# Optimization experiments

Measured on AMD Instinct MI355X. Metric: run time of the kernel, lower is better.

Reference implementation:

```python
import jax, jax.numpy as jnp
import numpy as np

RAD = 0.15          # sphere radius (init kwarg)
MIN_DIST = 2.0 * RAD  # two spheres collide when center distance < 2*rad


def setup_inputs() -> dict:
    key = jax.random.key(0)
    pos = jax.random.normal(key, (64, 1024, 3), dtype=jnp.float32)  # [T, N, 3]
    return {"pos": pos}


def reference(pos):
    """Sphere collision check equivalent to the sweep-and-prune CUDA kernel.

    The CUDA kernel sorts along one axis purely as an acceleration structure;
    the math it computes is: over all unordered robot pairs (i<j) at each
    timestep, a pair collides if ||p_i - p_j|| < 2*rad. Returns
      count: total number of colliding pairs (int)
      loss:  sum over colliding pairs of (2*rad - dist)^2 penetration penalty
    """
    T, N, _ = pos.shape
    diff = pos[:, :, None, :] - pos[:, None, :, :]          # [T, N, N, 3]
    dist2 = jnp.sum(diff * diff, axis=-1)                   # [T, N, N]
    iu = jnp.triu(jnp.ones((N, N), dtype=bool), k=1)        # i < j, exclude self
    colliding = iu[None, :, :] & (dist2 < MIN_DIST * MIN_DIST)
    # safe sqrt (diagonal / coincident points have dist2 == 0)
    safe_d2 = jnp.where(dist2 > 0.0, dist2, 1.0)
    dist = jnp.sqrt(safe_d2)
    pen = MIN_DIST - dist                                   # penetration depth
    loss = jnp.sum(jnp.where(colliding, pen * pen, 0.0))
    count = jnp.sum(colliding).astype(jnp.int32)
    return (count, loss)
```

## Files before the change

kernel.cpp:

```cpp
#include <hip/hip_runtime.h>
#include <math.h>

#define TN     64
#define NP     1024
#define RADIUS 0.15f
#define MIN_D  (2.0f * RADIUS)
#define R2     (MIN_D * MIN_D)

#define BLOCK  512
#define WAVES  (BLOCK / 64)
#define SPLIT  8
#define GI     16
#define NGRP   (NP / GI)
#define NBLK   (TN * SPLIT)
#define PPT    (NP / BLOCK)

#define NB     40
#define XMIN   (-6.0f)
#define INVW   3.3f

__launch_bounds__(BLOCK, 4)
__global__ void collide_kernel(const float* __restrict__ pos,
                               double* __restrict__ partial) {
    __shared__ float         shin[NP * 3];
    __shared__ float         shs [NP * 3];
    __shared__ unsigned int  hist[NB];
    __shared__ unsigned int  S[NB + 1];
    __shared__ unsigned char sbin[NP];

    const int t     = blockIdx.x / SPLIT;
    const int split = blockIdx.x % SPLIT;
    const int tid   = threadIdx.x;
    const int lane  = tid & 63;
    const int wave  = tid >> 6;

    const float4* p4  = (const float4*)(pos + (size_t)t * NP * 3);
    float4*       sh4 = (float4*)shin;
    for (int i = tid; i < NP * 3 / 4; i += BLOCK) sh4[i] = p4[i];
    if (tid < NB) hist[tid] = 0u;
    __syncthreads();

    int          bq[PPT];
    unsigned int rq[PPT];
    #pragma unroll
    for (int q = 0; q < PPT; ++q) {
        const int p = tid + q * BLOCK;
        const float x = shin[3 * p];
        int b = (int)((x - XMIN) * INVW);
        b = b < 0 ? 0 : (b > NB - 1 ? NB - 1 : b);
        bq[q] = b;
        rq[q] = atomicAdd(&hist[b], 1u);
    }
    __syncthreads();

    if (tid < 64) {
        unsigned int c    = (tid < NB) ? hist[tid] : 0u;
        unsigned int incl = c;
        #pragma unroll
        for (int d = 1; d < 64; d <<= 1) {
            const unsigned int y = __shfl_up(incl, d, 64);
            if (lane >= d) incl += y;
        }
        if (tid < NB) S[tid + 1] = incl;
        if (tid == 0) S[0] = 0u;
    }
    __syncthreads();

    #pragma unroll
    for (int q = 0; q < PPT; ++q) {
        const int p = tid + q * BLOCK;
        const unsigned int dst = S[bq[q]] + rq[q];
        shs[3 * dst + 0] = shin[3 * p + 0];
        shs[3 * dst + 1] = shin[3 * p + 1];
        shs[3 * dst + 2] = shin[3 * p + 2];
        sbin[dst] = (unsigned char)bq[q];
    }
    __syncthreads();

    unsigned int cnt  = 0;
    double       loss = 0.0;
    {
        const int g = wave * SPLIT + split;
        const int b = g * GI;

        float xi[GI], yi[GI], zi[GI];
        #pragma unroll
        for (int k = 0; k < GI; ++k) {
            xi[k] = shs[3 * (b + k) + 0];
            yi[k] = shs[3 * (b + k) + 1];
            zi[k] = shs[3 * (b + k) + 2];
        }
        #pragma unroll
        for (int k = 0; k < GI; ++k)
            asm volatile("" : "+v"(xi[k]), "+v"(yi[k]), "+v"(zi[k]));

        const int bb   = (int)sbin[b + GI - 1];
        const int jend = (int)S[(bb + 2 <= NB) ? (bb + 2) : NB];

        if (lane < GI - 1) {
            const int j = b + 1 + lane;
            const float xj = shs[3 * j], yj = shs[3 * j + 1], zj = shs[3 * j + 2];
            #pragma unroll
            for (int k = 0; k < GI; ++k) {
                if (k <= lane) {
                    const float dx = xi[k] - xj;
                    const float dy = yi[k] - yj;
                    const float dz = zi[k] - zj;
                    const float d2 = dx * dx + dy * dy + dz * dz;
                    if (d2 < R2) {
                        cnt++;
                        const float pen = MIN_D - __builtin_amdgcn_sqrtf(d2);
                        loss += (double)(pen * pen);
                    }
                }
            }
        }

        for (int j = b + GI + lane; j < jend; j += 64) {
            const float xj = shs[3 * j], yj = shs[3 * j + 1], zj = shs[3 * j + 2];
            #pragma unroll
            for (int k = 0; k < GI; ++k) {
                const float dx = xi[k] - xj;
                const float dy = yi[k] - yj;
                const float dz = zi[k] - zj;
                const float d2 = dx * dx + dy * dy + dz * dz;
                const bool hit = d2 < R2;
                cnt += hit ? 1u : 0u;
                if (hit) {
                    const float pen = MIN_D - __builtin_amdgcn_sqrtf(d2);
                    loss += (double)(pen * pen);
                }
            }
        }
    }

    float fcnt = (float)cnt;
    #pragma unroll
    for (int off = 32; off > 0; off >>= 1) {
        fcnt += __shfl_down(fcnt, off);
        loss += __shfl_down(loss, off);
    }
    __shared__ double cs[WAVES], ls[WAVES];
    if (lane == 0) { cs[wave] = (double)fcnt; ls[wave] = loss; }
    __syncthreads();
    if (tid == 0) {
        double c = 0.0, l = 0.0;
        #pragma unroll
        for (int w = 0; w < WAVES; ++w) { c += cs[w]; l += ls[w]; }
        partial[2 * blockIdx.x + 0] = c;
        partial[2 * blockIdx.x + 1] = l;
    }
}

__global__ void finalize_kernel(const double* __restrict__ partial,
                                float* __restrict__ out) {
    const int tid = threadIdx.x;
    double c = 0.0, l = 0.0;
    #pragma unroll
    for (int i = 0; i < NBLK / 256; ++i) {
        const double2 p = ((const double2*)partial)[tid + i * 256];
        c += p.x;
        l += p.y;
    }
    #pragma unroll
    for (int off = 32; off > 0; off >>= 1) {
        c += __shfl_down(c, off);
        l += __shfl_down(l, off);
    }
    __shared__ double cs[4], ls[4];
    const int wave = tid >> 6;
    if ((tid & 63) == 0) { cs[wave] = c; ls[wave] = l; }
    __syncthreads();
    if (tid == 0) {
        double ct = 0.0, lt = 0.0;
        #pragma unroll
        for (int w = 0; w < 4; ++w) { ct += cs[w]; lt += ls[w]; }
        out[0] = (float)ct;
        out[1] = (float)lt;
    }
}

extern "C" void kernel_launch(void* const* d_in, const int* in_sizes, int n_in,
                              void* d_out, int out_size, void* d_ws, size_t ws_size,
                              hipStream_t stream) {
    const float* pos     = (const float*)d_in[0];
    double*      partial = (double*)d_ws;
    float*       out     = (float*)d_out;

    collide_kernel<<<NBLK, BLOCK, 0, stream>>>(pos, partial);
    finalize_kernel<<<1, 256, 0, stream>>>(partial, out);
}
```

Measured before the change: 65.36 us.

## Use float accumulation, load positions into registers, and shrink finalize kernel

Loss is now accumulated in float instead of double, and the block and final reductions run in float. The input staging through a shared-memory buffer is removed: each thread loads its points straight from global memory into registers and scatters them into the sorted array. The distance computation uses explicit FMAs, and the finalize kernel becomes a single wave. The aim is to avoid slow FP64 adds and an extra shared-memory round trip, at the cost of reduced accumulation precision and uncoalesced strided global loads.

```diff
diff --git a/kernel.cpp b/kernel.cpp
--- a/kernel.cpp
+++ b/kernel.cpp
@@ -19,10 +19,13 @@
 #define XMIN   (-6.0f)
 #define INVW   3.3f
 
+__device__ __forceinline__ float dist2(float dx, float dy, float dz) {
+    return __builtin_fmaf(dx, dx, __builtin_fmaf(dy, dy, dz * dz));
+}
+
 __launch_bounds__(BLOCK, 4)
 __global__ void collide_kernel(const float* __restrict__ pos,
-                               double* __restrict__ partial) {
-    __shared__ float         shin[NP * 3];
+                               float* __restrict__ partial) {
     __shared__ float         shs [NP * 3];
     __shared__ unsigned int  hist[NB];
     __shared__ unsigned int  S[NB + 1];
@@ -34,19 +37,23 @@
     const int lane  = tid & 63;
     const int wave  = tid >> 6;
 
-    const float4* p4  = (const float4*)(pos + (size_t)t * NP * 3);
-    float4*       sh4 = (float4*)shin;
-    for (int i = tid; i < NP * 3 / 4; i += BLOCK) sh4[i] = p4[i];
-    if (tid < NB) hist[tid] = 0u;
-    __syncthreads();
-
+    const float* pt = pos + (size_t)t * NP * 3;
+    float px[PPT], py[PPT], pz[PPT];
     int          bq[PPT];
     unsigned int rq[PPT];
     #pragma unroll
     for (int q = 0; q < PPT; ++q) {
         const int p = tid + q * BLOCK;
-        const float x = shin[3 * p];
-        int b = (int)((x - XMIN) * INVW);
+        px[q] = pt[3 * p + 0];
+        py[q] = pt[3 * p + 1];
+        pz[q] = pt[3 * p + 2];
+    }
+    if (tid < NB) hist[tid] = 0u;
+    __syncthreads();
+
+    #pragma unroll
+    for (int q = 0; q < PPT; ++q) {
+        int b = (int)((px[q] - XMIN) * INVW);
         b = b < 0 ? 0 : (b > NB - 1 ? NB - 1 : b);
         bq[q] = b;
         rq[q] = atomicAdd(&hist[b], 1u);
@@ -68,17 +75,16 @@
 
     #pragma unroll
     for (int q = 0; q < PPT; ++q) {
-        const int p = tid + q * BLOCK;
         const unsigned int dst = S[bq[q]] + rq[q];
-        shs[3 * dst + 0] = shin[3 * p + 0];
-        shs[3 * dst + 1] = shin[3 * p + 1];
-        shs[3 * dst + 2] = shin[3 * p + 2];
+        shs[3 * dst + 0] = px[q];
+        shs[3 * dst + 1] = py[q];
+        shs[3 * dst + 2] = pz[q];
         sbin[dst] = (unsigned char)bq[q];
     }
     __syncthreads();
 
     unsigned int cnt  = 0;
-    double       loss = 0.0;
+    float        loss = 0.0f;
     {
         const int g = wave * SPLIT + split;
         const int b = g * GI;
@@ -103,14 +109,11 @@
             #pragma unroll
             for (int k = 0; k < GI; ++k) {
                 if (k <= lane) {
-                    const float dx = xi[k] - xj;
-                    const float dy = yi[k] - yj;
-                    const float dz = zi[k] - zj;
-                    const float d2 = dx * dx + dy * dy + dz * dz;
+                    const float d2 = dist2(xi[k] - xj, yi[k] - yj, zi[k] - zj);
                     if (d2 < R2) {
                         cnt++;
                         const float pen = MIN_D - __builtin_amdgcn_sqrtf(d2);
-                        loss += (double)(pen * pen);
+                        loss += pen * pen;
                     }
                 }
             }
@@ -120,15 +123,12 @@
             const float xj = shs[3 * j], yj = shs[3 * j + 1], zj = shs[3 * j + 2];
             #pragma unroll
             for (int k = 0; k < GI; ++k) {
-                const float dx = xi[k] - xj;
-                const float dy = yi[k] - yj;
-                const float dz = zi[k] - zj;
-                const float d2 = dx * dx + dy * dy + dz * dz;
+                const float d2 = dist2(xi[k] - xj, yi[k] - yj, zi[k] - zj);
                 const bool hit = d2 < R2;
                 cnt += hit ? 1u : 0u;
                 if (hit) {
                     const float pen = MIN_D - __builtin_amdgcn_sqrtf(d2);
-                    loss += (double)(pen * pen);
+                    loss += pen * pen;
                 }
             }
         }
@@ -140,11 +140,11 @@
         fcnt += __shfl_down(fcnt, off);
         loss += __shfl_down(loss, off);
     }
-    __shared__ double cs[WAVES], ls[WAVES];
-    if (lane == 0) { cs[wave] = (double)fcnt; ls[wave] = loss; }
+    __shared__ float cs[WAVES], ls[WAVES];
+    if (lane == 0) { cs[wave] = fcnt; ls[wave] = loss; }
     __syncthreads();
     if (tid == 0) {
-        double c = 0.0, l = 0.0;
+        float c = 0.0f, l = 0.0f;
         #pragma unroll
         for (int w = 0; w < WAVES; ++w) { c += cs[w]; l += ls[w]; }
         partial[2 * blockIdx.x + 0] = c;
@@ -152,13 +152,13 @@
     }
 }
 
-__global__ void finalize_kernel(const double* __restrict__ partial,
+__global__ void finalize_kernel(const float* __restrict__ partial,
                                 float* __restrict__ out) {
-    const int tid = threadIdx.x;
-    double c = 0.0, l = 0.0;
+    const int lane = threadIdx.x;
+    float c = 0.0f, l = 0.0f;
     #pragma unroll
-    for (int i = 0; i < NBLK / 256; ++i) {
-        const double2 p = ((const double2*)partial)[tid + i * 256];
+    for (int i = 0; i < NBLK / 64; ++i) {
+        const float2 p = ((const float2*)partial)[lane + i * 64];
         c += p.x;
         l += p.y;
     }
@@ -167,16 +167,9 @@
         c += __shfl_down(c, off);
         l += __shfl_down(l, off);
     }
-    __shared__ double cs[4], ls[4];
-    const int wave = tid >> 6;
-    if ((tid & 63) == 0) { cs[wave] = c; ls[wave] = l; }
-    __syncthreads();
-    if (tid == 0) {
-        double ct = 0.0, lt = 0.0;
-        #pragma unroll
-        for (int w = 0; w < 4; ++w) { ct += cs[w]; lt += ls[w]; }
-        out[0] = (float)ct;
-        out[1] = (float)lt;
+    if (lane == 0) {
+        out[0] = c;
+        out[1] = l;
     }
 }
 
@@ -184,9 +177,9 @@
                               void* d_out, int out_size, void* d_ws, size_t ws_size,
                               hipStream_t stream) {
     const float* pos     = (const float*)d_in[0];
-    double*      partial = (double*)d_ws;
+    float*       partial = (float*)d_ws;
     float*       out     = (float*)d_out;
 
     collide_kernel<<<NBLK, BLOCK, 0, stream>>>(pos, partial);
-    finalize_kernel<<<1, 256, 0, stream>>>(partial, out);
+    finalize_kernel<<<1, 64, 0, stream>>>(partial, out);
 }
```

Measured after the change: 63.51 us. 1.03x faster.
